# Performance work log

Hardware: AMD Instinct MI355X
Metric: run time of the kernel (lower is better)

The kernel has to match this reference:

```python
import jax, jax.numpy as jnp
import numpy as np

BITS = 4
PACK = 32 // BITS            # 8 nibbles per int32
IN, OUT = 4096, 4096
NNZ = 75008


def setup_inputs() -> dict:
    key = jax.random.key(0)
    ks = jax.random.split(key, 7)
    x = jax.random.normal(ks[0], (4, 2048, IN), jnp.float32)
    # packed 4-bit indices: any int32 bit pattern is valid after masking
    qweight = jax.random.randint(ks[1], (IN // PACK, OUT), 0, 2147483647, jnp.int32)
    lookup_table = jax.random.normal(ks[2], (OUT, 2 ** BITS), jnp.float32)
    bias = jax.random.normal(ks[3], (OUT,), jnp.float32)
    rows = jnp.sort(jax.random.randint(ks[4], (OUT + 1,), 0, NNZ, jnp.int32))
    outlier_rows = rows.at[0].set(0).at[-1].set(NNZ)  # valid CSR crow
    outlier_cols = jax.random.randint(ks[5], (NNZ,), 0, IN, jnp.int32)
    outlier_vals = jax.random.normal(ks[6], (NNZ,), jnp.float32)
    return {
        'x': x,
        'lookup_table': lookup_table,
        'bias': bias,
        'outlier_vals': outlier_vals,
        'qweight': qweight,
        'outlier_rows': outlier_rows,
        'outlier_cols': outlier_cols,
    }


def _dequant_weight(qweight, lookup_table):
    # unpack 8 4-bit indices per int32 along the packed-infeatures axis
    shifts = (jnp.arange(PACK, dtype=jnp.int32) * BITS)
    idx = ((qweight[:, None, :] >> shifts[None, :, None]) & 0xF)  # [IN//8, 8, OUT]
    idx = idx.reshape(IN, OUT)                                     # [IN, OUT]
    # per-output-channel LUT gather: W[o, i] = lut[o, idx[i, o]]
    return jnp.take_along_axis(lookup_table, idx.T, axis=1)       # [OUT, IN]


def reference(x, lookup_table, bias, outlier_vals, qweight, outlier_rows, outlier_cols):
    W = _dequant_weight(qweight, lookup_table)
    # CSR outlier correction: scatter-add sparse values into the dense weight
    row_ids = jnp.clip(
        jnp.searchsorted(outlier_rows, jnp.arange(NNZ, dtype=jnp.int32), side='right') - 1,
        0, OUT - 1)
    W = W.at[row_ids, outlier_cols].add(outlier_vals)
    x2 = x.reshape(-1, IN)
    y = x2 @ W.T + bias                                            # [B, OUT]
    return y.reshape(x.shape[:-1] + (OUT,))
```

## Files before the change

kernel.cpp:

```cpp
#include <hip/hip_runtime.h>
#include <stdint.h>

#define IN_F  4096
#define OUT_F 4096

typedef unsigned short u16;
typedef __attribute__((ext_vector_type(8))) short bf16x8;
typedef __attribute__((ext_vector_type(4))) float f32x4;

__device__ __forceinline__ u16 f2bf(float f) {
    union { float f; unsigned u; } c; c.f = f;
    unsigned u = c.u;
    return (u16)((u + 0x7FFFu + ((u >> 16) & 1u)) >> 16);
}
__device__ __forceinline__ float bf2f(u16 h) {
    union { unsigned u; float f; } c; c.u = ((unsigned)h) << 16;
    return c.f;
}

__device__ __forceinline__ void load_lds16(const void* g, void* l) {
    unsigned loff = (unsigned)(uintptr_t)l;
    loff = (unsigned)__builtin_amdgcn_readfirstlane((int)loff);
    __builtin_amdgcn_global_load_lds(
        (const __attribute__((address_space(1))) void*)(uintptr_t)g,
        (__attribute__((address_space(3))) void*)(uintptr_t)loff,
        16, 0, 0);
}

#define DQ_O 64
#define DQ_I 256

__global__ __launch_bounds__(256) void dequant_k(const int* __restrict__ qw,
                                                 const float* __restrict__ lut,
                                                 const int* __restrict__ rows,
                                                 const int* __restrict__ cols,
                                                 const float* __restrict__ vals,
                                                 u16* __restrict__ W) {
    __shared__ __align__(16) u16 sW[DQ_O * DQ_I];
    __shared__ u16 slut[DQ_O * 18];

    const int tid = threadIdx.x;
    const int o0 = blockIdx.y * DQ_O;
    const int i0 = blockIdx.x * DQ_I;
    const int p0 = i0 >> 3;

    {
        const int idx = tid * 4;
        const float4 v = *(const float4*)(lut + (size_t)o0 * 16 + idx);
        u16* d = slut + (idx >> 4) * 18 + (idx & 15);
        d[0] = f2bf(v.x); d[1] = f2bf(v.y); d[2] = f2bf(v.z); d[3] = f2bf(v.w);
    }
    __syncthreads();

    const int o_l = tid & 63;
    const int swz = o_l & 31;
#pragma unroll
    for (int it = 0; it < 8; ++it) {
        const int p = (tid >> 6) + it * 4;
        const unsigned w = (unsigned)qw[(size_t)(p0 + p) * OUT_F + (o0 + o_l)];
        union { u16 h[8]; uint4 v; } u;
#pragma unroll
        for (int j = 0; j < 8; ++j)
            u.h[j] = slut[o_l * 18 + ((w >> (4 * j)) & 15u)];
        *(uint4*)(sW + o_l * DQ_I + ((p ^ swz) << 3)) = u.v;
    }
    __syncthreads();

    if (tid < DQ_O) {
        const int s = rows[o0 + tid], e = rows[o0 + tid + 1];
        for (int k = s; k < e; ++k) {
            const unsigned j = (unsigned)(cols[k] - i0);
            if (j < DQ_I) {
                u16* p16 = sW + tid * DQ_I + (((j >> 3) ^ swz) << 3) + (j & 7);
                *p16 = f2bf(bf2f(*p16) + vals[k]);
            }
        }
    }
    __syncthreads();

    const int ch = tid & 31;
#pragma unroll
    for (int it = 0; it < 8; ++it) {
        const int r = (tid >> 5) + it * 8;
        *(uint4*)(W + (size_t)(o0 + r) * IN_F + i0 + ch * 8) =
            *(const uint4*)(sW + r * DQ_I + ((ch ^ (r & 31)) << 3));
    }
}

__global__ __launch_bounds__(256) void cvtx_k(const float4* __restrict__ x,
                                              u16* __restrict__ xb) {
    const size_t i = (size_t)blockIdx.x * 256 + threadIdx.x;
    const float4 a = x[2 * i];
    const float4 b = x[2 * i + 1];
    union { u16 h[8]; uint4 v; } u;
    u.h[0] = f2bf(a.x); u.h[1] = f2bf(a.y); u.h[2] = f2bf(a.z); u.h[3] = f2bf(a.w);
    u.h[4] = f2bf(b.x); u.h[5] = f2bf(b.y); u.h[6] = f2bf(b.z); u.h[7] = f2bf(b.w);
    *(uint4*)(xb + i * 8) = u.v;
}

#define GK 4096

#define MF(A_, B_, C_) __builtin_amdgcn_mfma_f32_16x16x32_bf16(A_, B_, C_, 0, 0, 0)

#define ROW(M_, AV)                                   \
    acc[M_][0] = MF(AV, b0, acc[M_][0]);              \
    acc[M_][1] = MF(AV, b1, acc[M_][1]);              \
    acc[M_][2] = MF(AV, b2, acc[M_][2]);              \
    acc[M_][3] = MF(AV, b3, acc[M_][3]);

#define STAGE_A(SLOT, KC) do {                                              \
    load_lds16(srcA0 + (KC) * 64, ldsA + (SLOT) * 16384 + ldst);            \
    load_lds16(srcA1 + (KC) * 64, ldsA + (SLOT) * 16384 + 8192 + ldst);     \
  } while (0)
#define STAGE_B(SLOT, KC) do {                                              \
    load_lds16(srcB0 + (KC) * 64, ldsB + (SLOT) * 16384 + ldst);            \
    load_lds16(srcB1 + (KC) * 64, ldsB + (SLOT) * 16384 + 8192 + ldst);     \
  } while (0)

#define WAIT4 asm volatile("s_waitcnt vmcnt(4)" ::: "memory")
#define VNOP  ((void)0)

#define PH_LO(SLOT, STAGE, WAIT)                                            \
  { const char* pa = ldsA + (SLOT) * 16384;                                 \
    const char* pb = ldsB + (SLOT) * 16384;                                 \
    a0 = *(const bf16x8*)(pa + offA0);                                      \
    a1 = *(const bf16x8*)(pa + offA1);                                      \
    a2 = *(const bf16x8*)(pa + offA2);                                      \
    a3 = *(const bf16x8*)(pa + offA3);                                      \
    b0 = *(const bf16x8*)(pb + offB0);                                      \
    b1 = *(const bf16x8*)(pb + offB1);                                      \
    b2 = *(const bf16x8*)(pb + offB2);                                      \
    b3 = *(const bf16x8*)(pb + offB3);                                      \
    STAGE;                                                                  \
    __builtin_amdgcn_s_barrier();                                           \
    asm volatile("s_waitcnt lgkmcnt(0)" ::: "memory");                      \
    __builtin_amdgcn_s_setprio(1);                                          \
    ROW(0, a0) ROW(1, a1) ROW(2, a2) ROW(3, a3)                             \
    __builtin_amdgcn_s_setprio(0);                                          \
    WAIT;                                                                   \
    __builtin_amdgcn_s_barrier(); }

#define PH_HI(SLOT, STAGE, WAIT)                                            \
  { const char* pa = ldsA + (SLOT) * 16384;                                 \
    a0 = *(const bf16x8*)(pa + offA4);                                      \
    a1 = *(const bf16x8*)(pa + offA5);                                      \
    a2 = *(const bf16x8*)(pa + offA6);                                      \
    a3 = *(const bf16x8*)(pa + offA7);                                      \
    STAGE;                                                                  \
    __builtin_amdgcn_s_barrier();                                           \
    asm volatile("s_waitcnt lgkmcnt(0)" ::: "memory");                      \
    __builtin_amdgcn_s_setprio(1);                                          \
    ROW(4, a0) ROW(5, a1) ROW(6, a2) ROW(7, a3)                             \
    __builtin_amdgcn_s_setprio(0);                                          \
    WAIT;                                                                   \
    __builtin_amdgcn_s_barrier(); }

__global__ __launch_bounds__(512, 2) void gemm8_k(const u16* __restrict__ A,
                                                  const u16* __restrict__ B,
                                                  const float* __restrict__ bias,
                                                  float* __restrict__ C,
                                                  int M, int N) {
    __shared__ __align__(16) u16 sAq[4 * 256 * 32];
    __shared__ __align__(16) u16 sBq[4 * 256 * 32];

    const int tid  = threadIdx.x;
    const int wave = tid >> 6;
    const int lane = tid & 63;

    const int ntx = N >> 8;
    const int nwg = (M >> 8) * ntx;
    const int cpx = nwg >> 3;
    const int bid = blockIdx.x;
    const int wg  = (bid & 7) * cpx + (bid >> 3);
    const int bm = (wg / ntx) << 8;
    const int bn = (wg % ntx) << 8;

    const int r4  = tid >> 2;
    const int cbs = ((tid & 3) << 4) ^ (((r4 >> 1) & 3) << 4);
    const char* srcA0 = (const char*)A + ((size_t)(bm + r4) * GK) * 2 + cbs;
    const char* srcA1 = (const char*)A + ((size_t)(bm + 128 + r4) * GK) * 2 + cbs;
    const char* srcB0 = (const char*)B + ((size_t)(bn + r4) * GK) * 2 + cbs;
    const char* srcB1 = (const char*)B + ((size_t)(bn + 128 + r4) * GK) * 2 + cbs;

    char* ldsA = (char*)sAq;
    char* ldsB = (char*)sBq;
    const int ldst = wave << 10;

    const int frow = lane & 15;
    const int fk2  = (lane >> 4) << 4;
    const int wmr  = (wave >> 2) << 7;
    const int wnr  = (wave & 3) << 6;
#define AOFF(m_) ((((wmr + (m_) * 16 + frow)) << 6) + \
                  (fk2 ^ ((((wmr + (m_) * 16 + frow) >> 1) & 3) << 4)))
#define BOFF(n_) ((((wnr + (n_) * 16 + frow)) << 6) + \
                  (fk2 ^ ((((wnr + (n_) * 16 + frow) >> 1) & 3) << 4)))
    const int offA0 = AOFF(0), offA1 = AOFF(1), offA2 = AOFF(2), offA3 = AOFF(3);
    const int offA4 = AOFF(4), offA5 = AOFF(5), offA6 = AOFF(6), offA7 = AOFF(7);
    const int offB0 = BOFF(0), offB1 = BOFF(1), offB2 = BOFF(2), offB3 = BOFF(3);
#undef AOFF
#undef BOFF

    f32x4 acc[8][4] = {};
    bf16x8 a0, a1, a2, a3, b0, b1, b2, b3;

    STAGE_A(0, 0); STAGE_B(0, 0);
    STAGE_A(1, 1); STAGE_B(1, 1);
    STAGE_A(2, 2); STAGE_B(2, 2);
    WAIT4;
    __builtin_amdgcn_s_barrier();

    for (int it = 0; it < 32; ++it) {
        const int c   = it * 4;
        const int kc3 = c + 3;
        const int kc4 = (c + 4) & 127;
        const int kc5 = (c + 5) & 127;
        const int kc6 = (c + 6) & 127;

        PH_LO(0, STAGE_A(3, kc3), VNOP)
        PH_HI(0, STAGE_B(3, kc3), VNOP)
        PH_LO(1, STAGE_A(0, kc4), VNOP)
        PH_HI(1, STAGE_B(0, kc4), WAIT4)
        PH_LO(2, STAGE_A(1, kc5), VNOP)
        PH_HI(2, STAGE_B(1, kc5), VNOP)
        PH_LO(3, STAGE_A(2, kc6), VNOP)
        PH_HI(3, STAGE_B(2, kc6), WAIT4)
    }

    const int cm = bm + wmr;
    const int cn = bn + wnr;
#pragma unroll
    for (int n = 0; n < 4; ++n) {
        const int col = cn + n * 16 + frow;
        const float bv = bias[col];
#pragma unroll
        for (int m = 0; m < 8; ++m) {
            const int r0 = cm + m * 16 + (lane >> 4) * 4;
#pragma unroll
            for (int r = 0; r < 4; ++r)
                C[(size_t)(r0 + r) * N + col] = acc[m][n][r] + bv;
        }
    }
}

extern "C" void kernel_launch(void* const* d_in, const int* in_sizes, int n_in,
                              void* d_out, int out_size, void* d_ws, size_t ws_size,
                              hipStream_t stream) {
    (void)n_in; (void)out_size; (void)ws_size;
    const float* x     = (const float*)d_in[0];
    const float* lut   = (const float*)d_in[1];
    const float* bias  = (const float*)d_in[2];
    const float* ovals = (const float*)d_in[3];
    const int*   qw    = (const int*)d_in[4];
    const int*   orows = (const int*)d_in[5];
    const int*   ocols = (const int*)d_in[6];
    float* y = (float*)d_out;

    const int M = in_sizes[0] / IN_F;

    u16* W  = (u16*)d_ws;
    u16* xb = (u16*)((char*)d_ws + (size_t)OUT_F * IN_F * 2);

    dim3 dq_grid(IN_F / DQ_I, OUT_F / DQ_O);
    dequant_k<<<dq_grid, 256, 0, stream>>>(qw, lut, orows, ocols, ovals, W);
    cvtx_k<<<(size_t)M * IN_F / 8 / 256, 256, 0, stream>>>((const float4*)x, xb);

    const int nwg = (M / 256) * (OUT_F / 256);
    gemm8_k<<<dim3(nwg), dim3(512), 0, stream>>>(xb, W, bias, y, M, OUT_F);
}
```

Baseline: 497.8 us.

## Merge dequant and x-convert kernels; software-pipeline LDS fragment reads in GEMM

Combines the weight dequant kernel and the x-to-bf16 conversion kernel into one launch, with a block-index split, which removes one launch and lets both run concurrently. The outlier loop is unrolled by four so the column and value loads can be issued together. The GEMM main loop is restructured so LDS fragment reads for the next phase are issued before the current phase's MFMAs, using double-buffered A/B register sets. This drops one barrier and the explicit lgkmcnt wait per phase, at the cost of more VGPRs, which may hurt occupancy at 2 waves per SIMD. It also relies on the compiler inserting correct waits.

Result: faster. 471.6 us (-5.3%).

```diff
diff --git a/kernel.cpp b/kernel.cpp
--- a/kernel.cpp
+++ b/kernel.cpp
@@ -29,19 +29,34 @@
 
 #define DQ_O 64
 #define DQ_I 256
-
-__global__ __launch_bounds__(256) void dequant_k(const int* __restrict__ qw,
-                                                 const float* __restrict__ lut,
-                                                 const int* __restrict__ rows,
-                                                 const int* __restrict__ cols,
-                                                 const float* __restrict__ vals,
-                                                 u16* __restrict__ W) {
+#define DQ_BLOCKS ((IN_F / DQ_I) * (OUT_F / DQ_O))
+
+__global__ __launch_bounds__(256) void prep_k(const int* __restrict__ qw,
+                                              const float* __restrict__ lut,
+                                              const int* __restrict__ rows,
+                                              const int* __restrict__ cols,
+                                              const float* __restrict__ vals,
+                                              u16* __restrict__ W,
+                                              const float4* __restrict__ x,
+                                              u16* __restrict__ xb) {
     __shared__ __align__(16) u16 sW[DQ_O * DQ_I];
     __shared__ u16 slut[DQ_O * 18];
 
     const int tid = threadIdx.x;
-    const int o0 = blockIdx.y * DQ_O;
-    const int i0 = blockIdx.x * DQ_I;
+
+    if (blockIdx.x >= DQ_BLOCKS) {
+        const size_t i = (size_t)(blockIdx.x - DQ_BLOCKS) * 256 + tid;
+        const float4 a = x[2 * i];
+        const float4 b = x[2 * i + 1];
+        union { u16 h[8]; uint4 v; } u;
+        u.h[0] = f2bf(a.x); u.h[1] = f2bf(a.y); u.h[2] = f2bf(a.z); u.h[3] = f2bf(a.w);
+        u.h[4] = f2bf(b.x); u.h[5] = f2bf(b.y); u.h[6] = f2bf(b.z); u.h[7] = f2bf(b.w);
+        *(uint4*)(xb + i * 8) = u.v;
+        return;
+    }
+
+    const int o0 = (blockIdx.x >> 4) * DQ_O;
+    const int i0 = (blockIdx.x & 15) * DQ_I;
     const int p0 = i0 >> 3;
 
     {
@@ -68,13 +83,20 @@
 
     if (tid < DQ_O) {
         const int s = rows[o0 + tid], e = rows[o0 + tid + 1];
-        for (int k = s; k < e; ++k) {
-            const unsigned j = (unsigned)(cols[k] - i0);
-            if (j < DQ_I) {
-                u16* p16 = sW + tid * DQ_I + (((j >> 3) ^ swz) << 3) + (j & 7);
-                *p16 = f2bf(bf2f(*p16) + vals[k]);
-            }
+        int k = s;
+#define APPLY(CJ, VV) do {                                                  \
+        const unsigned j_ = (unsigned)((CJ) - i0);                          \
+        if (j_ < DQ_I) {                                                    \
+            u16* p16 = sW + tid * DQ_I + (((j_ >> 3) ^ swz) << 3) + (j_ & 7); \
+            *p16 = f2bf(bf2f(*p16) + (VV));                                 \
+        } } while (0)
+        for (; k + 4 <= e; k += 4) {
+            const int c0 = cols[k], c1 = cols[k + 1], c2 = cols[k + 2], c3 = cols[k + 3];
+            const float v0 = vals[k], v1 = vals[k + 1], v2 = vals[k + 2], v3 = vals[k + 3];
+            APPLY(c0, v0); APPLY(c1, v1); APPLY(c2, v2); APPLY(c3, v3);
         }
+        for (; k < e; ++k) APPLY(cols[k], vals[k]);
+#undef APPLY
     }
     __syncthreads();
 
@@ -87,26 +109,9 @@
     }
 }
 
-__global__ __launch_bounds__(256) void cvtx_k(const float4* __restrict__ x,
-                                              u16* __restrict__ xb) {
-    const size_t i = (size_t)blockIdx.x * 256 + threadIdx.x;
-    const float4 a = x[2 * i];
-    const float4 b = x[2 * i + 1];
-    union { u16 h[8]; uint4 v; } u;
-    u.h[0] = f2bf(a.x); u.h[1] = f2bf(a.y); u.h[2] = f2bf(a.z); u.h[3] = f2bf(a.w);
-    u.h[4] = f2bf(b.x); u.h[5] = f2bf(b.y); u.h[6] = f2bf(b.z); u.h[7] = f2bf(b.w);
-    *(uint4*)(xb + i * 8) = u.v;
-}
-
 #define GK 4096
 
 #define MF(A_, B_, C_) __builtin_amdgcn_mfma_f32_16x16x32_bf16(A_, B_, C_, 0, 0, 0)
-
-#define ROW(M_, AV)                                   \
-    acc[M_][0] = MF(AV, b0, acc[M_][0]);              \
-    acc[M_][1] = MF(AV, b1, acc[M_][1]);              \
-    acc[M_][2] = MF(AV, b2, acc[M_][2]);              \
-    acc[M_][3] = MF(AV, b3, acc[M_][3]);
 
 #define STAGE_A(SLOT, KC) do {                                              \
     load_lds16(srcA0 + (KC) * 64, ldsA + (SLOT) * 16384 + ldst);            \
@@ -120,39 +125,39 @@
 #define WAIT4 asm volatile("s_waitcnt vmcnt(4)" ::: "memory")
 #define VNOP  ((void)0)
 
-#define PH_LO(SLOT, STAGE, WAIT)                                            \
-  { const char* pa = ldsA + (SLOT) * 16384;                                 \
-    const char* pb = ldsB + (SLOT) * 16384;                                 \
-    a0 = *(const bf16x8*)(pa + offA0);                                      \
-    a1 = *(const bf16x8*)(pa + offA1);                                      \
-    a2 = *(const bf16x8*)(pa + offA2);                                      \
-    a3 = *(const bf16x8*)(pa + offA3);                                      \
-    b0 = *(const bf16x8*)(pb + offB0);                                      \
-    b1 = *(const bf16x8*)(pb + offB1);                                      \
-    b2 = *(const bf16x8*)(pb + offB2);                                      \
-    b3 = *(const bf16x8*)(pb + offB3);                                      \
-    STAGE;                                                                  \
-    __builtin_amdgcn_s_barrier();                                           \
-    asm volatile("s_waitcnt lgkmcnt(0)" ::: "memory");                      \
+#define LDA(S, M) (*(const bf16x8*)(ldsA + (S) * 16384 + (M) * 1024 + aoff))
+#define LDB(S, N) (*(const bf16x8*)(ldsB + (S) * 16384 + (N) * 1024 + boff))
+
+#define RD_ALO(S) aA0 = LDA(S, 0); aA1 = LDA(S, 1); aA2 = LDA(S, 2); aA3 = LDA(S, 3)
+#define RD_AHI(S) aB0 = LDA(S, 4); aB1 = LDA(S, 5); aB2 = LDA(S, 6); aB3 = LDA(S, 7)
+#define RD_BA(S)  bA0 = LDB(S, 0); bA1 = LDB(S, 1); bA2 = LDB(S, 2); bA3 = LDB(S, 3)
+#define RD_BB(S)  bB0 = LDB(S, 0); bB1 = LDB(S, 1); bB2 = LDB(S, 2); bB3 = LDB(S, 3)
+
+#define MFMA16(A0, A1, A2, A3, B0, B1, B2, B3, R)                           \
+    acc[(R)+0][0] = MF(A0, B0, acc[(R)+0][0]);                              \
+    acc[(R)+0][1] = MF(A0, B1, acc[(R)+0][1]);                              \
+    acc[(R)+0][2] = MF(A0, B2, acc[(R)+0][2]);                              \
+    acc[(R)+0][3] = MF(A0, B3, acc[(R)+0][3]);                              \
+    acc[(R)+1][0] = MF(A1, B0, acc[(R)+1][0]);                              \
+    acc[(R)+1][1] = MF(A1, B1, acc[(R)+1][1]);                              \
+    acc[(R)+1][2] = MF(A1, B2, acc[(R)+1][2]);                              \
+    acc[(R)+1][3] = MF(A1, B3, acc[(R)+1][3]);                              \
+    acc[(R)+2][0] = MF(A2, B0, acc[(R)+2][0]);                              \
+    acc[(R)+2][1] = MF(A2, B1, acc[(R)+2][1]);                              \
+    acc[(R)+2][2] = MF(A2, B2, acc[(R)+2][2]);                              \
+    acc[(R)+2][3] = MF(A2, B3, acc[(R)+2][3]);                              \
+    acc[(R)+3][0] = MF(A3, B0, acc[(R)+3][0]);                              \
+    acc[(R)+3][1] = MF(A3, B1, acc[(R)+3][1]);                              \
+    acc[(R)+3][2] = MF(A3, B2, acc[(R)+3][2]);                              \
+    acc[(R)+3][3] = MF(A3, B3, acc[(R)+3][3]);
+
+#define PHASE(RDNEXT, STG, A0, A1, A2, A3, B0, B1, B2, B3, R, VM)           \
+  { RDNEXT;                                                                 \
+    STG;                                                                    \
     __builtin_amdgcn_s_setprio(1);                                          \
-    ROW(0, a0) ROW(1, a1) ROW(2, a2) ROW(3, a3)                             \
+    MFMA16(A0, A1, A2, A3, B0, B1, B2, B3, R)                               \
     __builtin_amdgcn_s_setprio(0);                                          \
-    WAIT;                                                                   \
-    __builtin_amdgcn_s_barrier(); }
-
-#define PH_HI(SLOT, STAGE, WAIT)                                            \
-  { const char* pa = ldsA + (SLOT) * 16384;                                 \
-    a0 = *(const bf16x8*)(pa + offA4);                                      \
-    a1 = *(const bf16x8*)(pa + offA5);                                      \
-    a2 = *(const bf16x8*)(pa + offA6);                                      \
-    a3 = *(const bf16x8*)(pa + offA7);                                      \
-    STAGE;                                                                  \
-    __builtin_amdgcn_s_barrier();                                           \
-    asm volatile("s_waitcnt lgkmcnt(0)" ::: "memory");                      \
-    __builtin_amdgcn_s_setprio(1);                                          \
-    ROW(4, a0) ROW(5, a1) ROW(6, a2) ROW(7, a3)                             \
-    __builtin_amdgcn_s_setprio(0);                                          \
-    WAIT;                                                                   \
+    VM;                                                                     \
     __builtin_amdgcn_s_barrier(); }
 
 __global__ __launch_bounds__(512, 2) void gemm8_k(const u16* __restrict__ A,
@@ -188,26 +193,22 @@
 
     const int frow = lane & 15;
     const int fk2  = (lane >> 4) << 4;
+    const int fswz = ((frow >> 1) & 3) << 4;
     const int wmr  = (wave >> 2) << 7;
     const int wnr  = (wave & 3) << 6;
-#define AOFF(m_) ((((wmr + (m_) * 16 + frow)) << 6) + \
-                  (fk2 ^ ((((wmr + (m_) * 16 + frow) >> 1) & 3) << 4)))
-#define BOFF(n_) ((((wnr + (n_) * 16 + frow)) << 6) + \
-                  (fk2 ^ ((((wnr + (n_) * 16 + frow) >> 1) & 3) << 4)))
-    const int offA0 = AOFF(0), offA1 = AOFF(1), offA2 = AOFF(2), offA3 = AOFF(3);
-    const int offA4 = AOFF(4), offA5 = AOFF(5), offA6 = AOFF(6), offA7 = AOFF(7);
-    const int offB0 = BOFF(0), offB1 = BOFF(1), offB2 = BOFF(2), offB3 = BOFF(3);
-#undef AOFF
-#undef BOFF
+    const int aoff = ((wmr + frow) << 6) + (fk2 ^ fswz);
+    const int boff = ((wnr + frow) << 6) + (fk2 ^ fswz);
 
     f32x4 acc[8][4] = {};
-    bf16x8 a0, a1, a2, a3, b0, b1, b2, b3;
+    bf16x8 aA0, aA1, aA2, aA3, aB0, aB1, aB2, aB3;
+    bf16x8 bA0, bA1, bA2, bA3, bB0, bB1, bB2, bB3;
 
     STAGE_A(0, 0); STAGE_B(0, 0);
     STAGE_A(1, 1); STAGE_B(1, 1);
     STAGE_A(2, 2); STAGE_B(2, 2);
     WAIT4;
     __builtin_amdgcn_s_barrier();
+    RD_ALO(0); RD_BA(0);
 
     for (int it = 0; it < 32; ++it) {
         const int c   = it * 4;
@@ -216,14 +217,14 @@
         const int kc5 = (c + 5) & 127;
         const int kc6 = (c + 6) & 127;
 
-        PH_LO(0, STAGE_A(3, kc3), VNOP)
-        PH_HI(0, STAGE_B(3, kc3), VNOP)
-        PH_LO(1, STAGE_A(0, kc4), VNOP)
-        PH_HI(1, STAGE_B(0, kc4), WAIT4)
-        PH_LO(2, STAGE_A(1, kc5), VNOP)
-        PH_HI(2, STAGE_B(1, kc5), VNOP)
-        PH_LO(3, STAGE_A(2, kc6), VNOP)
-        PH_HI(3, STAGE_B(2, kc6), WAIT4)
+        PHASE(RD_AHI(0),            STAGE_A(3, kc3), aA0, aA1, aA2, aA3, bA0, bA1, bA2, bA3, 0, VNOP)
+        PHASE(RD_ALO(1); RD_BB(1),  STAGE_B(3, kc3), aB0, aB1, aB2, aB3, bA0, bA1, bA2, bA3, 4, WAIT4)
+        PHASE(RD_AHI(1),            STAGE_A(0, kc4), aA0, aA1, aA2, aA3, bB0, bB1, bB2, bB3, 0, VNOP)
+        PHASE(RD_ALO(2); RD_BA(2),  STAGE_B(0, kc4), aB0, aB1, aB2, aB3, bB0, bB1, bB2, bB3, 4, WAIT4)
+        PHASE(RD_AHI(2),            STAGE_A(1, kc5), aA0, aA1, aA2, aA3, bA0, bA1, bA2, bA3, 0, VNOP)
+        PHASE(RD_ALO(3); RD_BB(3),  STAGE_B(1, kc5), aB0, aB1, aB2, aB3, bA0, bA1, bA2, bA3, 4, WAIT4)
+        PHASE(RD_AHI(3),            STAGE_A(2, kc6), aA0, aA1, aA2, aA3, bB0, bB1, bB2, bB3, 0, VNOP)
+        PHASE(RD_ALO(0); RD_BA(0),  STAGE_B(2, kc6), aB0, aB1, aB2, aB3, bB0, bB1, bB2, bB3, 4, WAIT4)
     }
 
     const int cm = bm + wmr;
@@ -260,9 +261,9 @@
     u16* W  = (u16*)d_ws;
     u16* xb = (u16*)((char*)d_ws + (size_t)OUT_F * IN_F * 2);
 
-    dim3 dq_grid(IN_F / DQ_I, OUT_F / DQ_O);
-    dequant_k<<<dq_grid, 256, 0, stream>>>(qw, lut, orows, ocols, ovals, W);
-    cvtx_k<<<(size_t)M * IN_F / 8 / 256, 256, 0, stream>>>((const float4*)x, xb);
+    const int cvt_blocks = (int)((size_t)M * IN_F / 8 / 256);
+    prep_k<<<DQ_BLOCKS + cvt_blocks, 256, 0, stream>>>(
+        qw, lut, orows, ocols, ovals, W, (const float4*)x, xb);
 
     const int nwg = (M / 256) * (OUT_F / 256);
     gemm8_k<<<dim3(nwg), dim3(512), 0, stream>>>(xb, W, bias, y, M, OUT_F);
```
